# Optimization experiments

Hardware: AMD Instinct MI355X
Metric: run time of the kernel (lower is better)

The kernel has to match this reference:

```python
import jax, jax.numpy as jnp
import numpy as np

NUM_CLASSES = 80
IMG = 640
STRIDES = (8, 16, 32)
CENTER_RADIUS = 2.5
TOPK = 10  # n_candidate_k; dynamic_ks = clamp(int(sum top-10 IoU), 1) <= 10


def _make_grids():
    gs, ss = [], []
    for s in STRIDES:
        n = IMG // s
        gy, gx = np.meshgrid(np.arange(n), np.arange(n), indexing="ij")
        gs.append(np.stack([gx.ravel(), gy.ravel()], 1).astype(np.float32))
        ss.append(np.full(n * n, s, np.float32))
    return np.concatenate(gs, 0), np.concatenate(ss, 0)


def setup_inputs() -> dict:
    key = jax.random.key(0)
    B, T, C = 16, 128, NUM_CLASSES
    grid_np, stride_np = _make_grids()
    A = grid_np.shape[0]  # 8400
    k1, k2, k3, k4, k5, k6 = jax.random.split(key, 6)
    # pred boxes: plausible abs xyxy around anchor centers
    ctr = jnp.asarray((grid_np + 0.5) * stride_np[:, None])[None]
    ctr = ctr + 4.0 * jax.random.normal(k1, (B, A, 2))
    wh = jnp.asarray(stride_np)[None, :, None] * jax.random.uniform(k2, (B, A, 2), minval=1.0, maxval=4.0)
    box = jnp.concatenate([ctr - wh / 2, ctr + wh / 2], -1)
    logits = 2.0 * jax.random.normal(k3, (B, A, 1 + C))
    pred = jnp.concatenate([box, logits], -1)  # [B, A, 5+C]
    # targets: [B, T, 6] = (batch_id, cid, x1, y1, x2, y2)
    tc = jax.random.uniform(k4, (B, T, 2), minval=60.0, maxval=580.0)
    twh = jax.random.uniform(k5, (B, T, 2), minval=30.0, maxval=200.0)
    tbox = jnp.concatenate([tc - twh / 2, tc + twh / 2], -1)
    cid = jax.random.randint(k6, (B, T, 1), 0, C).astype(jnp.float32)
    bid = jnp.broadcast_to(jnp.arange(B, dtype=jnp.float32)[:, None, None], (B, T, 1))
    target = jnp.concatenate([bid, cid, tbox], -1)
    return {"pred": pred, "target": target,
            "grid_mask": jnp.asarray(grid_np), "stride_mask": jnp.asarray(stride_np)}


def _pairwise_iou(a, b):
    # a [T,4], b [A,4], xyxy -> [T,A]
    lt = jnp.maximum(a[:, None, :2], b[None, :, :2])
    rb = jnp.minimum(a[:, None, 2:], b[None, :, 2:])
    wh = jnp.clip(rb - lt, 0.0, None)
    inter = wh[..., 0] * wh[..., 1]
    area_a = jnp.clip(a[:, 2] - a[:, 0], 0.0, None) * jnp.clip(a[:, 3] - a[:, 1], 0.0, None)
    area_b = jnp.clip(b[:, 2] - b[:, 0], 0.0, None) * jnp.clip(b[:, 3] - b[:, 1], 0.0, None)
    return inter / (area_a[:, None] + area_b[None, :] - inter + 1e-8)


def _ciou(p, t):
    # complete IoU, elementwise over leading dims, xyxy
    lt = jnp.maximum(p[..., :2], t[..., :2])
    rb = jnp.minimum(p[..., 2:], t[..., 2:])
    wh = jnp.clip(rb - lt, 0.0, None)
    inter = wh[..., 0] * wh[..., 1]
    wp, hp = p[..., 2] - p[..., 0], p[..., 3] - p[..., 1]
    wt, ht = t[..., 2] - t[..., 0], t[..., 3] - t[..., 1]
    iou = inter / (wp * hp + wt * ht - inter + 1e-8)
    cwh = jnp.maximum(p[..., 2:], t[..., 2:]) - jnp.minimum(p[..., :2], t[..., :2])
    c2 = cwh[..., 0] ** 2 + cwh[..., 1] ** 2 + 1e-8
    rho2 = (((p[..., 0] + p[..., 2]) - (t[..., 0] + t[..., 2])) ** 2
            + ((p[..., 1] + p[..., 3]) - (t[..., 1] + t[..., 3])) ** 2) / 4.0
    v = (4.0 / jnp.pi ** 2) * (jnp.arctan(wt / (ht + 1e-8)) - jnp.arctan(wp / (hp + 1e-8))) ** 2
    alpha = v / (1.0 - iou + v + 1e-8)
    return iou - rho2 / c2 - alpha * v


def _bce_logits(x, t):
    return jnp.maximum(x, 0.0) - x * t + jnp.log1p(jnp.exp(-jnp.abs(x)))


def _assign_image(pred_i, tgt_i, grid, stride):
    # pred_i [A,5+C], tgt_i [T,6]
    A, T, C = pred_i.shape[0], tgt_i.shape[0], NUM_CLASSES
    tbox = tgt_i[:, 2:6]
    cid = tgt_i[:, 1].astype(jnp.int32)
    xc = (grid[:, 0] + 0.5) * stride  # [A]
    yc = (grid[:, 1] + 0.5) * stride
    d = jnp.stack([xc[None] - tbox[:, 0:1], yc[None] - tbox[:, 1:2],
                   tbox[:, 2:3] - xc[None], tbox[:, 3:4] - yc[None]], -1)  # [T,A,4]
    in_boxes = d.min(-1) > 0.0  # [T,A]
    txc = (tbox[:, 0] + tbox[:, 2]) / 2
    tyc = (tbox[:, 1] + tbox[:, 3]) / 2
    in_centers = jnp.maximum(jnp.abs(xc[None] - txc[:, None]),
                             jnp.abs(yc[None] - tyc[:, None])) < CENTER_RADIUS * stride[None]
    in_box = in_boxes.any(0) | in_centers.any(0)  # [A], candidate anchors
    in_box_center = in_boxes & in_centers  # [T,A]
    iou = jnp.where(in_box[None], _pairwise_iou(tbox, pred_i[:, :4]), 0.0)  # [T,A]
    iou_cost = -jnp.log(iou + 1e-8)
    prob = jnp.sqrt(jax.nn.sigmoid(pred_i[:, 4:5]) * jax.nn.sigmoid(pred_i[:, 5:]))  # [A,C]
    logp = jnp.maximum(jnp.log(prob), -100.0)      # torch BCE clamps log at -100
    log1mp = jnp.maximum(jnp.log1p(-prob), -100.0)
    # sum_c BCE(prob, onehot(cid)) computed analytically (avoids [T,A,C]):
    cls_cost = -(log1mp.sum(-1)[None, :] + (logp - log1mp)[:, cid].T)  # [T,A]
    # 1e9 keeps anchors outside in_box out of the candidate pool (original slices them away)
    cost = cls_cost + 3.0 * iou_cost + 1e5 * (~in_box_center) + 1e9 * (~in_box)[None, :]
    topk_ious, _ = jax.lax.top_k(iou, TOPK)  # [T,10]
    dyn_k = jnp.maximum(topk_ious.sum(1).astype(jnp.int32), 1)  # [T]
    _, idx = jax.lax.top_k(-cost, TOPK)  # 10 lowest-cost anchors per target
    sel = jnp.arange(TOPK)[None, :] < dyn_k[:, None]  # keep first dyn_k of them
    matching = jnp.zeros((T, A), bool).at[jnp.arange(T)[:, None], idx].set(sel)
    matching = matching & in_box[None, :]
    conflict = matching.sum(0) > 1  # anchors claimed by >1 targets
    keep = jnp.arange(T)[:, None] == jnp.argmin(cost, 0)[None, :]  # [T,A]
    matching = jnp.where(conflict[None, :], keep, matching)
    mp = matching.any(0)  # [A]
    tp = jnp.argmax(matching, 0)  # [A] target index per anchor
    p_iou = jnp.clip((iou / (iou.max(1, keepdims=True) + 1e-8)).max(0), 0.0, 1.0)  # [A]
    obj_t = jnp.where(in_box, p_iou, 0.0)
    box_t = tbox[tp]  # [A,4]
    cls_t = jax.nn.one_hot(cid[tp], C, dtype=jnp.float32)  # [A,C]
    return mp, box_t, obj_t, cls_t


def reference(pred, target, grid_mask, stride_mask):
    B, A = pred.shape[:2]
    C = NUM_CLASSES
    mp, box_t, obj_t, cls_t = jax.lax.stop_gradient(
        jax.vmap(_assign_image, in_axes=(0, 0, None, None))(pred, target, grid_mask, stride_mask))
    m = mp.reshape(-1).astype(pred.dtype)  # matched-anchor mask over B*A
    n = jnp.maximum(m.sum(), 1.0)
    p = pred.reshape(B * A, -1)
    lbox = 0.05 * jnp.sum((1.0 - _ciou(p[:, :4], box_t.reshape(-1, 4))) * m) / n
    lobj = _bce_logits(p[:, 4], obj_t.reshape(-1)).mean()
    lcls = 0.5 * jnp.sum(_bce_logits(p[:, 5:], cls_t.reshape(-1, C)).mean(-1) * m) / n
    loss = lbox + lobj + lcls
    return loss, jnp.stack([lbox, lobj, lcls])
```

## Files before the change

### kernel.cpp

```cpp
#include <hip/hip_runtime.h>
#include <cfloat>

#pragma clang fp contract(off)

#define NCLS 80
#define PDIM 85
#define NA   8400
#define NAP  8448
#define NB   16
#define NT   128
#define NTOP 10
#define APB  64
#define BPI  132
#define BPI2 33
#define LN2  0.6931471805599453f
#define CAPW 768

#define BAPC ((size_t)NB*NAP)

#define KSENT 0xFFFFFFFF7FFFFFFFull

__device__ __forceinline__ float sigm_fast(float x){
  float e = __expf(-x);
  return __builtin_amdgcn_rcpf(1.0f + e);
}

__device__ __forceinline__ float bce_fast(float x, float t){
  float ax = fabsf(x);
  float e  = __expf(-ax);
  return fmaxf(x,0.0f) - x*t + LN2*__builtin_amdgcn_logf(1.0f + e);
}

__device__ __forceinline__ float pair_iou(float tx1,float ty1,float tx2,float ty2,
                                          float px1,float py1,float px2,float py2){
  float w = fminf(tx2,px2) - fmaxf(tx1,px1);
  float h = fminf(ty2,py2) - fmaxf(ty1,py1);
  w = fmaxf(w,0.0f); h = fmaxf(h,0.0f);
  float inter = w*h;
  float at = fmaxf(tx2-tx1,0.0f)*fmaxf(ty2-ty1,0.0f);
  float ap = fmaxf(px2-px1,0.0f)*fmaxf(py2-py1,0.0f);
  float den = at+ap-inter+1e-8f;
  return inter * __builtin_amdgcn_rcpf(den);
}

__device__ __forceinline__ float dval_fn(float sobj, float lg){
  float ln_sobj = LN2*__builtin_amdgcn_logf(sobj);
  float e = __expf(-fabsf(lg));
  float L = LN2*__builtin_amdgcn_logf(1.0f + e);
  float ln_sc = -(fmaxf(-lg,0.0f) + L);
  float lph = 0.5f*(ln_sobj + ln_sc);
  float p = __expf(lph);
  float lp = fmaxf(lph, -100.0f);
  float l1 = fmaxf(LN2*__builtin_amdgcn_logf(fmaxf(1.0f - p, 0.0f)), -100.0f);
  return lp - l1;
}

__device__ __forceinline__ float cost_from(float S, float dval, float iou, bool ibc, bool ib){
  float iouc = -LN2 * __builtin_amdgcn_logf(iou + 1e-8f);
  float clsc = -(S + dval);
  float c = clsc + 3.0f*iouc;
  c = c + (ibc ? 0.0f : 100000.0f);
  c = c + (ib  ? 0.0f : 1000000000.0f);
  return c;
}

__device__ __forceinline__ unsigned long long key_of(float c, int idx){
  unsigned int u = __float_as_uint(c);
  u ^= (u & 0x80000000u) ? 0xFFFFFFFFu : 0x80000000u;
  return ((unsigned long long)u << 32) | (unsigned int)idx;
}

__device__ __forceinline__ void ins_iou(float* riou, float iou){
  if (iou > riou[NTOP-1]){
    #pragma unroll
    for (int j = NTOP-1; j >= 1; --j){
      bool gj  = iou > riou[j];
      bool gj1 = iou > riou[j-1];
      riou[j] = gj ? (gj1 ? riou[j-1] : iou) : riou[j];
    }
    riou[0] = (iou > riou[0]) ? iou : riou[0];
  }
}
__device__ __forceinline__ void ins_key(unsigned long long* rk, unsigned long long key){
  if (key < rk[NTOP-1]){
    #pragma unroll
    for (int j = NTOP-1; j >= 1; --j){
      bool bj  = key < rk[j];
      bool bj1 = key < rk[j-1];
      rk[j] = bj ? (bj1 ? rk[j-1] : key) : rk[j];
    }
    rk[0] = (key < rk[0]) ? key : rk[0];
  }
}

__global__ __launch_bounds__(256) void k0_precompute(
    const float* __restrict__ pred, const float* __restrict__ target,
    const float* __restrict__ grid, const float* __restrict__ stridev,
    float4* __restrict__ pbox4, float4* __restrict__ meta4,
    float* __restrict__ obja, float* __restrict__ sobja,
    float* __restrict__ S0a, float* __restrict__ D, int use_d,
    unsigned long long* __restrict__ mask, unsigned int* __restrict__ obju,
    float4* __restrict__ gaabb, unsigned long long* __restrict__ actm,
    float* __restrict__ acc)
{
  __shared__ __align__(16) float tile[APB*PDIM];
  __shared__ float4 tb4s[NT];
  __shared__ float  ps_s[4][APB];
  __shared__ float  ps0_s[4][APB];
  __shared__ int    ib_s[4][APB];

  int i  = blockIdx.x / BPI;
  int b  = blockIdx.x % BPI;
  int c0 = b*APB;
  int n  = NA - c0; if (n > APB) n = APB;
  int tid = threadIdx.x;

  if (blockIdx.x == 0) acc[tid] = 0.0f;

  const float4* src4 = (const float4*)(pred + ((size_t)i*NA + c0)*PDIM);
  int tot4 = (n*PDIM) >> 2;
  for (int idx = tid; idx < tot4; idx += 256) ((float4*)tile)[idx] = src4[idx];
  for (int idx = tid; idx < NT; idx += 256){
    const float* tg = target + (i*NT + idx)*6;
    tb4s[idx] = make_float4(tg[2],tg[3],tg[4],tg[5]);
  }
  __syncthreads();

  int al = tid & 63, cg = tid >> 6;
  if (al < n){
    int gid = i*NAP + c0 + al;
    float x4 = tile[al*PDIM+4];
    float e4 = __expf(-fabsf(x4));
    float L4 = LN2*__builtin_amdgcn_logf(1.0f + e4);
    float ln_sobj = -(fmaxf(-x4,0.0f) + L4);
    float ps = 0.0f, ps0 = 0.0f;
    #pragma unroll 4
    for (int k = 0; k < 20; ++k){
      int c = cg*20 + k;
      float x  = tile[al*PDIM+5+c];
      float e  = __expf(-fabsf(x));
      float L  = LN2*__builtin_amdgcn_logf(1.0f + e);
      float ln_sc = -(fmaxf(-x,0.0f) + L);
      float lph = 0.5f*(ln_sobj + ln_sc);
      float p   = __expf(lph);
      float lp  = fmaxf(lph, -100.0f);
      float l1  = fmaxf(LN2*__builtin_amdgcn_logf(fmaxf(1.0f - p, 0.0f)), -100.0f);
      ps  += l1;
      if (use_d) D[(size_t)c*BAPC + gid] = lp - l1;
      ps0 += fmaxf(x,0.0f) + L;
    }
    ps_s[cg][al] = ps; ps0_s[cg][al] = ps0;

    int ga = c0 + al;
    float xg = grid[2*ga], yg = grid[2*ga+1], sv = stridev[ga];
    float xc = (xg + 0.5f)*sv, yc = (yg + 0.5f)*sv;
    float rc = 2.5f*sv;
    bool ibp = false;
    #pragma unroll 4
    for (int t = cg*32; t < cg*32+32; ++t){
      float4 T = tb4s[t];
      bool inb = (xc-T.x>0.0f)&&(yc-T.y>0.0f)&&(T.z-xc>0.0f)&&(T.w-yc>0.0f);
      float txc=(T.x+T.z)*0.5f, tyc=(T.y+T.w)*0.5f;
      bool inc = fmaxf(fabsf(xc-txc),fabsf(yc-tyc)) < rc;
      ibp = ibp || inb || inc;
    }
    ib_s[cg][al] = ibp ? 1 : 0;
  }
  __syncthreads();

  if (tid < APB){
    int a = tid;
    bool real = (a < n);
    int gid = i*NAP + c0 + a;
    float x1=0,y1=0,x2=0,y2=0,xc=0,yc=0,rc=0;
    bool ib = false;

    if (real){
      float s  = ps_s[0][a]  + ps_s[1][a]  + ps_s[2][a]  + ps_s[3][a];
      float s0 = ps0_s[0][a] + ps0_s[1][a] + ps0_s[2][a] + ps0_s[3][a];
      ib  = (ib_s[0][a] | ib_s[1][a] | ib_s[2][a] | ib_s[3][a]) != 0;

      x1 = tile[a*PDIM+0]; y1 = tile[a*PDIM+1];
      x2 = tile[a*PDIM+2]; y2 = tile[a*PDIM+3];
      float ol = tile[a*PDIM+4];
      pbox4[gid] = make_float4(x1,y1,x2,y2);
      obja[gid]  = ol;
      sobja[gid] = sigm_fast(ol);
      S0a[gid]   = s0;
      mask[(size_t)gid*2]   = 0ull;
      mask[(size_t)gid*2+1] = 0ull;
      obju[gid] = 0u;

      int ga = c0 + a;
      float xg = grid[2*ga], yg = grid[2*ga+1], sv = stridev[ga];
      xc = (xg + 0.5f)*sv; yc = (yg + 0.5f)*sv;
      rc = 2.5f*sv;
      meta4[gid] = make_float4(xc, yc, ib ? rc : -rc, s);
    } else {
      meta4[gid] = make_float4(0.0f, 0.0f, -1.0f, 0.0f);
      pbox4[gid] = make_float4(0.0f, 0.0f, 0.0f, 0.0f);
      obju[gid]  = 0u;
    }

    bool iv = real && ib;
    unsigned long long am = __ballot(iv);
    float bx1 = iv ? x1 : FLT_MAX,  by1 = iv ? y1 : FLT_MAX;
    float bx2 = iv ? x2 : -FLT_MAX, by2 = iv ? y2 : -FLT_MAX;
    float cx1 = iv ? xc : FLT_MAX,  cy1 = iv ? yc : FLT_MAX;
    float cx2 = iv ? xc : -FLT_MAX, cy2 = iv ? yc : -FLT_MAX;
    float rx1 = iv ? xc-rc : FLT_MAX,  ry1 = iv ? yc-rc : FLT_MAX;
    float rx2 = iv ? xc+rc : -FLT_MAX, ry2 = iv ? yc+rc : -FLT_MAX;
    #pragma unroll
    for (int off = 32; off > 0; off >>= 1){
      bx1 = fminf(bx1, __shfl_xor(bx1, off));
      by1 = fminf(by1, __shfl_xor(by1, off));
      bx2 = fmaxf(bx2, __shfl_xor(bx2, off));
      by2 = fmaxf(by2, __shfl_xor(by2, off));
      cx1 = fminf(cx1, __shfl_xor(cx1, off));
      cy1 = fminf(cy1, __shfl_xor(cy1, off));
      cx2 = fmaxf(cx2, __shfl_xor(cx2, off));
      cy2 = fmaxf(cy2, __shfl_xor(cy2, off));
      rx1 = fminf(rx1, __shfl_xor(rx1, off));
      ry1 = fminf(ry1, __shfl_xor(ry1, off));
      rx2 = fmaxf(rx2, __shfl_xor(rx2, off));
      ry2 = fmaxf(ry2, __shfl_xor(ry2, off));
    }
    if (tid == 0){
      size_t gb = (size_t)(i*BPI + b)*3;
      gaabb[gb+0] = make_float4(bx1,by1,bx2,by2);
      gaabb[gb+1] = make_float4(cx1,cy1,cx2,cy2);
      gaabb[gb+2] = make_float4(rx1,ry1,rx2,ry2);
      actm[i*BPI + b] = am;
    }
  }
}

__global__ __launch_bounds__(256) void k1_pertarget(
    const float4* __restrict__ pbox4, const float4* __restrict__ meta4,
    const float* __restrict__ D, int use_d,
    const float* __restrict__ sobja, const float* __restrict__ pred,
    const float* __restrict__ target, const float4* __restrict__ gaabb,
    const unsigned long long* __restrict__ actm,
    unsigned int* __restrict__ obju, unsigned long long* __restrict__ mask)
{
  __shared__ int   seg[4*CAPW];
  __shared__ int   cnts_s[4], cibc_s[4];
  __shared__ float wiou[4][NTOP];
  __shared__ unsigned long long wkey[4][NTOP];
  __shared__ float rmax_s;

  int tid = threadIdx.x, lane = tid & 63, w = tid >> 6;
  int g = blockIdx.x;
  int i = g / NT, t = g - i*NT;
  int iNAP = i*NAP;
  int iNA  = i*NA;
  const float* m4f = (const float*)meta4;

  const float* tg = target + (size_t)g*6;
  int   cid = (int)tg[1];
  float tx1 = tg[2], ty1 = tg[3], tx2 = tg[4], ty2 = tg[5];
  float txc = (tx1+tx2)*0.5f, tyc = (ty1+ty2)*0.5f;
  const float* Dc = use_d ? (D + (size_t)cid*BAPC) : nullptr;

  bool sv = false, svi = false;
  if (lane < 33){
    size_t gb = (size_t)(i*BPI + (w + 4*lane))*3;
    float4 gbb = gaabb[gb+0];
    float4 gcc = gaabb[gb+1];
    float4 grr = gaabb[gb+2];
    bool ovg  = (fminf(tx2,gbb.z) > fmaxf(tx1,gbb.x)) &&
                (fminf(ty2,gbb.w) > fmaxf(ty1,gbb.y));
    bool inbg = (gcc.z > tx1) && (gcc.x < tx2) && (gcc.w > ty1) && (gcc.y < ty2);
    bool incg = (txc > grr.x) && (txc < grr.z) && (tyc > grr.y) && (tyc < grr.w);
    svi = inbg && incg;
    sv = ovg || svi;
  }
  unsigned long long gmsk  = __ballot(sv);
  unsigned long long gmski = __ballot(svi);

  int cnt = 0, ci = 0;
  while (gmsk){
    int k = __ffsll(gmsk) - 1;
    unsigned long long kb = 1ull << k;
    gmsk &= gmsk - 1;
    int a = w*64 + k*256 + lane;
    float4 pb = pbox4[iNAP+a];

    bool ov  = (fminf(tx2,pb.z) > fmaxf(tx1,pb.x)) &&
               (fminf(ty2,pb.w) > fmaxf(ty1,pb.y));

    if (gmski & kb){
      float4 mt = meta4[iNAP+a];
      bool act = (mt.z > 0.0f);
      bool inb = (mt.x-tx1>0.0f)&&(mt.y-ty1>0.0f)&&(tx2-mt.x>0.0f)&&(ty2-mt.y>0.0f);
      bool inc = fmaxf(fabsf(mt.x-txc),fabsf(mt.y-tyc)) < mt.z;
      bool ibc = inb && inc;
      bool cand = act && (ov || ibc);
      unsigned long long bb  = __ballot(cand);
      unsigned long long bb2 = __ballot(ibc);
      if (cand){
        int pos = cnt + __popcll(bb & ((1ull << lane) - 1ull));
        if (pos < CAPW) seg[w*CAPW + pos] = a | (ibc ? (1<<15) : 0);
      }
      cnt += __popcll(bb);
      ci  += __popcll(bb2);
    } else {
      unsigned long long am = actm[i*BPI + (w + 4*k)];
      bool act = (am >> lane) & 1ull;
      bool cand = act && ov;
      unsigned long long bb = __ballot(cand);
      if (cand){
        int pos = cnt + __popcll(bb & ((1ull << lane) - 1ull));
        if (pos < CAPW) seg[w*CAPW + pos] = a;
      }
      cnt += __popcll(bb);
    }
  }
  if (lane == 0){ cnts_s[w] = cnt; cibc_s[w] = ci; }
  __syncthreads();

  int tibc = cibc_s[0]+cibc_s[1]+cibc_s[2]+cibc_s[3];
  bool ovf = (cnts_s[0]>CAPW)||(cnts_s[1]>CAPW)||(cnts_s[2]>CAPW)||(cnts_s[3]>CAPW);
  bool fastp = !ovf && (tibc >= 16);

  float riou[NTOP]; unsigned long long rk[NTOP];
  #pragma unroll
  for (int j=0;j<NTOP;++j){ riou[j]=0.0f; rk[j]=KSENT; }

  int cw = cnts_s[w];
  if (fastp){
    for (int j = lane; j < cw; j += 64){
      int e  = seg[w*CAPW + j];
      int a1 = e & 0x3fff;
      bool ibc = (e & (1<<15)) != 0;
      int gid = iNAP + a1;
      float4 pb2 = pbox4[gid];
      float iou = pair_iou(tx1,ty1,tx2,ty2, pb2.x,pb2.y,pb2.z,pb2.w);
      ins_iou(riou, iou);
      float S  = m4f[(size_t)gid*4 + 3];
      float dv = use_d ? Dc[gid] : dval_fn(sobja[gid], pred[(size_t)(iNA+a1)*PDIM + 5 + cid]);
      float c  = cost_from(S, dv, iou, ibc, true);
      ins_key(rk, key_of(c, a1));
    }
  } else {
    for (int a1 = tid; a1 < NA; a1 += 256){
      float4 mt2 = meta4[iNAP+a1];
      if (mt2.z > 0.0f){
        float4 pb2 = pbox4[iNAP+a1];
        float iou = pair_iou(tx1,ty1,tx2,ty2, pb2.x,pb2.y,pb2.z,pb2.w);
        ins_iou(riou, iou);
        bool inb = (mt2.x-tx1>0.0f)&&(mt2.y-ty1>0.0f)&&(tx2-mt2.x>0.0f)&&(ty2-mt2.y>0.0f);
        bool inc = fmaxf(fabsf(mt2.x-txc),fabsf(mt2.y-tyc)) < mt2.z;
        float dv = use_d ? Dc[iNAP+a1] : dval_fn(sobja[iNAP+a1], pred[(size_t)(iNA+a1)*PDIM + 5 + cid]);
        float c = cost_from(mt2.w, dv, iou, inb&&inc, true);
        ins_key(rk, key_of(c, a1));
      }
    }
  }

  #pragma unroll
  for (int r = 0; r < NTOP; ++r){
    float gm = riou[0];
    #pragma unroll
    for (int m = 1; m < 64; m <<= 1) gm = fmaxf(gm, __shfl_xor(gm, m));
    unsigned long long bb = __ballot(riou[0] == gm);
    int win = __ffsll(bb) - 1;
    if (lane == win){
      #pragma unroll
      for (int j=0;j<NTOP-1;++j) riou[j] = riou[j+1];
      riou[NTOP-1] = 0.0f;
    }
    if (lane == 0) wiou[w][r] = gm;
  }
  #pragma unroll
  for (int r = 0; r < NTOP; ++r){
    unsigned long long gk = rk[0];
    #pragma unroll
    for (int m = 1; m < 64; m <<= 1){
      unsigned long long o = __shfl_xor(gk, m);
      gk = (o < gk) ? o : gk;
    }
    if (rk[0] == gk){
      #pragma unroll
      for (int j=0;j<NTOP-1;++j) rk[j] = rk[j+1];
      rk[NTOP-1] = KSENT;
    }
    if (lane == 0) wkey[w][r] = gk;
  }
  __syncthreads();

  int dk = 1;
  if (w == 0){
    int p0=0,p1=0,p2=0,p3=0;
    float ssum = 0.0f, rmax = 0.0f;
    #pragma unroll
    for (int r = 0; r < NTOP; ++r){
      float v0=wiou[0][p0], v1=wiou[1][p1], v2=wiou[2][p2], v3=wiou[3][p3];
      float mx = fmaxf(fmaxf(v0,v1), fmaxf(v2,v3));
      if (r == 0) rmax = mx;
      ssum += mx;
      if      (mx == v0) ++p0;
      else if (mx == v1) ++p1;
      else if (mx == v2) ++p2;
      else               ++p3;
    }
    dk = (int)ssum;
    if (dk < 1) dk = 1;
    if (lane == 0) rmax_s = rmax;
  }
  __syncthreads();

  float invm = 1.0f / (rmax_s + 1e-8f);
  if (fastp){
    for (int j = lane; j < cw; j += 64){
      int a1 = seg[w*CAPW + j] & 0x3fff;
      int gid = iNAP + a1;
      float4 pb2 = pbox4[gid];
      float iou = pair_iou(tx1,ty1,tx2,ty2, pb2.x,pb2.y,pb2.z,pb2.w);
      float v = iou * invm;
      if (v > 0.0f) atomicMax(&obju[gid], __float_as_uint(v));
    }
  } else {
    for (int a1 = tid; a1 < NA; a1 += 256){
      float4 mt2 = meta4[iNAP+a1];
      if (mt2.z > 0.0f){
        float4 pb2 = pbox4[iNAP+a1];
        float iou = pair_iou(tx1,ty1,tx2,ty2, pb2.x,pb2.y,pb2.z,pb2.w);
        float v = iou * invm;
        if (v > 0.0f) atomicMax(&obju[iNAP+a1], __float_as_uint(v));
      }
    }
  }

  if (w == 0){
    int q0=0,q1=0,q2=0,q3=0;
    int myidx = 0x7fffffff;
    #pragma unroll
    for (int r = 0; r < NTOP; ++r){
      unsigned long long k0=wkey[0][q0], k1=wkey[1][q1], k2=wkey[2][q2], k3=wkey[3][q3];
      unsigned long long mn = k0;
      mn = (k1 < mn) ? k1 : mn;
      mn = (k2 < mn) ? k2 : mn;
      mn = (k3 < mn) ? k3 : mn;
      if (lane == r) myidx = (int)(mn & 0xFFFFFFFFull);
      if      (mn == k0) ++q0;
      else if (mn == k1) ++q1;
      else if (mn == k2) ++q2;
      else               ++q3;
    }

    if (lane < NTOP && lane < dk){
      int a1 = myidx;
      if (a1 >= 0 && a1 < NA){
        atomicOr(&mask[(size_t)(iNAP + a1)*2 + (t>>6)], 1ull << (t & 63));
      }
    }
  }
}

__global__ __launch_bounds__(256) void k2_peranchor(
    const float* __restrict__ pred,
    const float4* __restrict__ pbox4, const float4* __restrict__ meta4,
    const float* __restrict__ obja, const float* __restrict__ sobja,
    const float* __restrict__ S0a,
    const float* __restrict__ D, int use_d,
    const float* __restrict__ target,
    const unsigned int* __restrict__ obju, const unsigned long long* __restrict__ mask,
    float* __restrict__ acc)
{
  __shared__ float4 tb4[NT];
  __shared__ int    tcid[NT];
  __shared__ int    cl[256];
  __shared__ int    bt_s[256];
  __shared__ int    ncl;
  __shared__ float4 part[4];

  int i  = blockIdx.x / BPI2;
  int b  = blockIdx.x - i*BPI2;
  int tid = threadIdx.x, lane = tid & 63, w = tid >> 6;
  int a  = b*256 + tid;
  int gid = i*NAP + a;

  if (tid < NT){
    const float* tg = target + (i*NT + tid)*6;
    tcid[tid] = (int)tg[1];
    tb4[tid]  = make_float4(tg[2],tg[3],tg[4],tg[5]);
  }
  if (tid == 0) ncl = 0;

  bool valid = (a < NA);
  float4 pb = pbox4[gid];
  float4 mt = meta4[gid];
  unsigned long long m0=0, m1=0;
  if (valid){ m0 = mask[(size_t)gid*2]; m1 = mask[(size_t)gid*2+1]; }
  float bestv = __uint_as_float(obju[gid]);
  float olv   = obja[gid];
  float S0v   = S0a[gid];

  bool ib = valid && (mt.z > 0.0f);
  float px1=pb.x, py1=pb.y, px2=pb.z, py2=pb.w;
  int cnt = __popcll(m0) + __popcll(m1);

  __syncthreads();

  bool myc = (cnt > 1);
  unsigned long long cb = __ballot(myc);
  int nb = __popcll(cb);
  int base = 0;
  if (lane == 0 && nb) base = atomicAdd(&ncl, nb);
  base = __shfl(base, 0);
  if (myc) cl[base + __popcll(cb & ((1ull << lane) - 1ull))] = tid;
  __syncthreads();

  int tot = ncl;
  for (int ci = w; ci < tot; ci += 4){
    int aidx = cl[ci];
    int a2g  = b*256 + aidx;
    int gid2 = i*NAP + a2g;
    float4 pb2 = pbox4[gid2];
    float4 mt2 = meta4[gid2];
    bool ib2 = (mt2.z > 0.0f);
    float rc2 = fabsf(mt2.z);
    float Sg  = mt2.w;
    float sobj = use_d ? 0.0f : sobja[gid2];
    size_t pbase = (size_t)(i*NA + a2g)*PDIM;

    int ta = lane, tb = lane + 64;
    float dva = use_d ? D[(size_t)tcid[ta]*BAPC + gid2]
                      : dval_fn(sobj, pred[pbase + 5 + tcid[ta]]);
    float dvb = use_d ? D[(size_t)tcid[tb]*BAPC + gid2]
                      : dval_fn(sobj, pred[pbase + 5 + tcid[tb]]);

    float4 Ta = tb4[ta];
    float ioua = ib2 ? pair_iou(Ta.x,Ta.y,Ta.z,Ta.w,pb2.x,pb2.y,pb2.z,pb2.w) : 0.0f;
    bool inba = (mt2.x-Ta.x>0.0f)&&(mt2.y-Ta.y>0.0f)&&(Ta.z-mt2.x>0.0f)&&(Ta.w-mt2.y>0.0f);
    float txa=(Ta.x+Ta.z)*0.5f, tya=(Ta.y+Ta.w)*0.5f;
    bool inca = fmaxf(fabsf(mt2.x-txa),fabsf(mt2.y-tya)) < rc2;
    unsigned long long ka = key_of(cost_from(Sg, dva, ioua, inba&&inca, ib2), ta);

    float4 Tb = tb4[tb];
    float ioub = ib2 ? pair_iou(Tb.x,Tb.y,Tb.z,Tb.w,pb2.x,pb2.y,pb2.z,pb2.w) : 0.0f;
    bool inbb = (mt2.x-Tb.x>0.0f)&&(mt2.y-Tb.y>0.0f)&&(Tb.z-mt2.x>0.0f)&&(Tb.w-mt2.y>0.0f);
    float txb=(Tb.x+Tb.z)*0.5f, tyb=(Tb.y+Tb.w)*0.5f;
    bool incb = fmaxf(fabsf(mt2.x-txb),fabsf(mt2.y-tyb)) < rc2;
    unsigned long long kb = key_of(cost_from(Sg, dvb, ioub, inbb&&incb, ib2), tb);

    unsigned long long mn = (kb < ka) ? kb : ka;
    #pragma unroll
    for (int m = 1; m < 64; m <<= 1){
      unsigned long long o = __shfl_xor(mn, m);
      mn = (o < mn) ? o : mn;
    }
    if (lane == 0) bt_s[aidx] = (int)(mn & 0xFFFFFFFFull);
  }
  __syncthreads();

  float m=0.0f, vbox=0.0f, vobj=0.0f, vcls=0.0f;
  if (valid){
    float obj_t = ib ? fminf(fmaxf(bestv,0.0f),1.0f) : 0.0f;
    vobj = bce_fast(olv, obj_t);

    int tp = 0; bool mpv = false;
    if (cnt > 1){ tp = bt_s[tid]; mpv = true; }
    else if (cnt == 1){
      tp = m0 ? (__ffsll(m0)-1) : (64 + __ffsll(m1)-1);
      mpv = true;
    }

    if (mpv){
      m = 1.0f;
      float4 T = tb4[tp];
      float x1=T.x, y1=T.y, x2=T.z, y2=T.w;
      float w2 = fmaxf(fminf(px2,x2)-fmaxf(px1,x1),0.0f);
      float h2 = fmaxf(fminf(py2,y2)-fmaxf(py1,y1),0.0f);
      float inter = w2*h2;
      float wp=px2-px1, hp=py2-py1, wt=x2-x1, ht=y2-y1;
      float iou = inter/(wp*hp + wt*ht - inter + 1e-8f);
      float cw = fmaxf(px2,x2)-fminf(px1,x1);
      float ch = fmaxf(py2,y2)-fminf(py1,y1);
      float c2 = cw*cw + ch*ch + 1e-8f;
      float dx = (px1+px2)-(x1+x2), dy = (py1+py2)-(y1+y2);
      float rho2 = (dx*dx + dy*dy)/4.0f;
      float da = atanf(wt/(ht+1e-8f)) - atanf(wp/(hp+1e-8f));
      float v  = 0.4052847345693511f * da * da;
      float alpha = v/(1.0f - iou + v + 1e-8f);
      vbox = 1.0f - (iou - rho2/c2 - alpha*v);

      int cc = tcid[tp];
      float xcc = pred[(size_t)(i*NA + a)*PDIM + 5 + cc];
      vcls = (S0v - xcc) * (1.0f/80.0f);
    }
  }

  #pragma unroll
  for (int off=32; off>0; off>>=1){
    m    += __shfl_down(m, off);
    vbox += __shfl_down(vbox, off);
    vobj += __shfl_down(vobj, off);
    vcls += __shfl_down(vcls, off);
  }
  if (lane == 0) part[w] = make_float4(m, vbox, vobj, vcls);
  __syncthreads();
  if (tid == 0){
    float4 s0 = part[0], s1 = part[1], s2 = part[2], s3 = part[3];
    float4 s = make_float4(s0.x+s1.x+s2.x+s3.x, s0.y+s1.y+s2.y+s3.y,
                           s0.z+s1.z+s2.z+s3.z, s0.w+s1.w+s2.w+s3.w);
    int slot = (blockIdx.x & 63)*4;
    atomicAdd(&acc[slot+0], s.x);
    atomicAdd(&acc[slot+1], s.y);
    atomicAdd(&acc[slot+2], s.z);
    atomicAdd(&acc[slot+3], s.w);
  }
}

__global__ void k3_final(const float* __restrict__ acc, float* __restrict__ out){
  int l = threadIdx.x;
  float4 v = ((const float4*)acc)[l];
  #pragma unroll
  for (int off=32; off>0; off>>=1){
    v.x += __shfl_down(v.x, off);
    v.y += __shfl_down(v.y, off);
    v.z += __shfl_down(v.z, off);
    v.w += __shfl_down(v.w, off);
  }
  if (l == 0){
    float n    = fmaxf(v.x, 1.0f);
    float lbox = 0.05f * v.y / n;
    float lobj = v.z / (float)(NB*NA);
    float lcls = 0.5f  * v.w / n;
    out[0] = lbox + lobj + lcls;
    out[1] = lbox; out[2] = lobj; out[3] = lcls;
  }
}

extern "C" void kernel_launch(void* const* d_in, const int* in_sizes, int n_in,
                              void* d_out, int out_size, void* d_ws, size_t ws_size,
                              hipStream_t stream) {
  const float* pred    = (const float*)d_in[0];
  const float* target  = (const float*)d_in[1];
  const float* grid    = (const float*)d_in[2];
  const float* stridev = (const float*)d_in[3];
  float* out = (float*)d_out;

  char* ws = (char*)d_ws;

  size_t off = 0;
  unsigned long long* mask = (unsigned long long*)(ws + off); off += BAPC*16;
  float* acc    = (float*)(ws + off); off += 64*4*4;
  float4* pbox4 = (float4*)(ws + off); off += BAPC*16;
  float4* meta4 = (float4*)(ws + off); off += BAPC*16;
  float* obja   = (float*)(ws + off); off += BAPC*4;
  float* sobja  = (float*)(ws + off); off += BAPC*4;
  float* S0a    = (float*)(ws + off); off += BAPC*4;
  unsigned int* obju = (unsigned int*)(ws + off); off += BAPC*4;
  float4* gaabb = (float4*)(ws + off); off += (size_t)NB*BPI*3*16;
  unsigned long long* actm = (unsigned long long*)(ws + off); off += (size_t)NB*BPI*8;
  float* D      = (float*)(ws + off);
  const size_t need_d = off + (size_t)NCLS*BAPC*4;
  int use_d = (ws_size >= need_d) ? 1 : 0;

  k0_precompute<<<NB*BPI, 256, 0, stream>>>(pred, target, grid, stridev,
                                            pbox4, meta4, obja, sobja, S0a, D, use_d,
                                            mask, obju, gaabb, actm, acc);
  k1_pertarget <<<NB*NT,  256, 0, stream>>>(pbox4, meta4, D, use_d,
                                            sobja, pred, target, gaabb, actm,
                                            obju, mask);
  k2_peranchor <<<NB*BPI2, 256, 0, stream>>>(pred, pbox4, meta4, obja, sobja, S0a,
                                             D, use_d, target, obju, mask, acc);
  k3_final     <<<1, 64, 0, stream>>>(acc, out);
}
```

Baseline: 152.6 us.

## Drop precomputed per-class D table and recompute cost terms on demand

Removes the large per-class D array that k0 wrote for every anchor and class (80×B×A floats) and the sigmoid-objectness buffer. k1 and k2 now recompute the class cost term from the raw objectness and class logit via a log-sigmoid formulation. k1 also caches the candidate IoU in shared memory (int2 segment) so the second pass skips reloading boxes and recomputing IoU, with the per-warp capacity reduced from 768 to 512 to keep shared memory in check. This trades large global writes for extra transcendental math, and the smaller capacity may push more targets onto the slow path.

```diff
diff --git a/kernel.cpp b/kernel.cpp
--- a/kernel.cpp
+++ b/kernel.cpp
@@ -14,16 +14,11 @@
 #define BPI  132
 #define BPI2 33
 #define LN2  0.6931471805599453f
-#define CAPW 768
+#define CAPW 512
 
 #define BAPC ((size_t)NB*NAP)
 
 #define KSENT 0xFFFFFFFF7FFFFFFFull
-
-__device__ __forceinline__ float sigm_fast(float x){
-  float e = __expf(-x);
-  return __builtin_amdgcn_rcpf(1.0f + e);
-}
 
 __device__ __forceinline__ float bce_fast(float x, float t){
   float ax = fabsf(x);
@@ -43,15 +38,17 @@
   return inter * __builtin_amdgcn_rcpf(den);
 }
 
-__device__ __forceinline__ float dval_fn(float sobj, float lg){
-  float ln_sobj = LN2*__builtin_amdgcn_logf(sobj);
-  float e = __expf(-fabsf(lg));
-  float L = LN2*__builtin_amdgcn_logf(1.0f + e);
+__device__ __forceinline__ float dval_exact(float ol, float lg){
+  float e4 = __expf(-fabsf(ol));
+  float L4 = LN2*__builtin_amdgcn_logf(1.0f + e4);
+  float ln_sobj = -(fmaxf(-ol,0.0f) + L4);
+  float e  = __expf(-fabsf(lg));
+  float L  = LN2*__builtin_amdgcn_logf(1.0f + e);
   float ln_sc = -(fmaxf(-lg,0.0f) + L);
   float lph = 0.5f*(ln_sobj + ln_sc);
-  float p = __expf(lph);
-  float lp = fmaxf(lph, -100.0f);
-  float l1 = fmaxf(LN2*__builtin_amdgcn_logf(fmaxf(1.0f - p, 0.0f)), -100.0f);
+  float p   = __expf(lph);
+  float lp  = fmaxf(lph, -100.0f);
+  float l1  = fmaxf(LN2*__builtin_amdgcn_logf(fmaxf(1.0f - p, 0.0f)), -100.0f);
   return lp - l1;
 }
 
@@ -97,8 +94,7 @@
     const float* __restrict__ pred, const float* __restrict__ target,
     const float* __restrict__ grid, const float* __restrict__ stridev,
     float4* __restrict__ pbox4, float4* __restrict__ meta4,
-    float* __restrict__ obja, float* __restrict__ sobja,
-    float* __restrict__ S0a, float* __restrict__ D, int use_d,
+    float* __restrict__ obja, float* __restrict__ S0a,
     unsigned long long* __restrict__ mask, unsigned int* __restrict__ obju,
     float4* __restrict__ gaabb, unsigned long long* __restrict__ actm,
     float* __restrict__ acc)
@@ -128,7 +124,6 @@
 
   int al = tid & 63, cg = tid >> 6;
   if (al < n){
-    int gid = i*NAP + c0 + al;
     float x4 = tile[al*PDIM+4];
     float e4 = __expf(-fabsf(x4));
     float L4 = LN2*__builtin_amdgcn_logf(1.0f + e4);
@@ -143,10 +138,8 @@
       float ln_sc = -(fmaxf(-x,0.0f) + L);
       float lph = 0.5f*(ln_sobj + ln_sc);
       float p   = __expf(lph);
-      float lp  = fmaxf(lph, -100.0f);
       float l1  = fmaxf(LN2*__builtin_amdgcn_logf(fmaxf(1.0f - p, 0.0f)), -100.0f);
       ps  += l1;
-      if (use_d) D[(size_t)c*BAPC + gid] = lp - l1;
       ps0 += fmaxf(x,0.0f) + L;
     }
     ps_s[cg][al] = ps; ps0_s[cg][al] = ps0;
@@ -185,7 +178,6 @@
       float ol = tile[a*PDIM+4];
       pbox4[gid] = make_float4(x1,y1,x2,y2);
       obja[gid]  = ol;
-      sobja[gid] = sigm_fast(ol);
       S0a[gid]   = s0;
       mask[(size_t)gid*2]   = 0ull;
       mask[(size_t)gid*2+1] = 0ull;
@@ -237,13 +229,12 @@
 
 __global__ __launch_bounds__(256) void k1_pertarget(
     const float4* __restrict__ pbox4, const float4* __restrict__ meta4,
-    const float* __restrict__ D, int use_d,
-    const float* __restrict__ sobja, const float* __restrict__ pred,
+    const float* __restrict__ obja, const float* __restrict__ pred,
     const float* __restrict__ target, const float4* __restrict__ gaabb,
     const unsigned long long* __restrict__ actm,
     unsigned int* __restrict__ obju, unsigned long long* __restrict__ mask)
 {
-  __shared__ int   seg[4*CAPW];
+  __shared__ int2  seg2[4*CAPW];
   __shared__ int   cnts_s[4], cibc_s[4];
   __shared__ float wiou[4][NTOP];
   __shared__ unsigned long long wkey[4][NTOP];
@@ -260,7 +251,6 @@
   int   cid = (int)tg[1];
   float tx1 = tg[2], ty1 = tg[3], tx2 = tg[4], ty2 = tg[5];
   float txc = (tx1+tx2)*0.5f, tyc = (ty1+ty2)*0.5f;
-  const float* Dc = use_d ? (D + (size_t)cid*BAPC) : nullptr;
 
   bool sv = false, svi = false;
   if (lane < 33){
@@ -300,7 +290,7 @@
       unsigned long long bb2 = __ballot(ibc);
       if (cand){
         int pos = cnt + __popcll(bb & ((1ull << lane) - 1ull));
-        if (pos < CAPW) seg[w*CAPW + pos] = a | (ibc ? (1<<15) : 0);
+        if (pos < CAPW) seg2[w*CAPW + pos].x = a | (ibc ? (1<<15) : 0);
       }
       cnt += __popcll(bb);
       ci  += __popcll(bb2);
@@ -311,7 +301,7 @@
       unsigned long long bb = __ballot(cand);
       if (cand){
         int pos = cnt + __popcll(bb & ((1ull << lane) - 1ull));
-        if (pos < CAPW) seg[w*CAPW + pos] = a;
+        if (pos < CAPW) seg2[w*CAPW + pos].x = a;
       }
       cnt += __popcll(bb);
     }
@@ -330,15 +320,16 @@
   int cw = cnts_s[w];
   if (fastp){
     for (int j = lane; j < cw; j += 64){
-      int e  = seg[w*CAPW + j];
+      int e  = seg2[w*CAPW + j].x;
       int a1 = e & 0x3fff;
       bool ibc = (e & (1<<15)) != 0;
       int gid = iNAP + a1;
       float4 pb2 = pbox4[gid];
       float iou = pair_iou(tx1,ty1,tx2,ty2, pb2.x,pb2.y,pb2.z,pb2.w);
+      seg2[w*CAPW + j].y = __float_as_int(iou);
       ins_iou(riou, iou);
       float S  = m4f[(size_t)gid*4 + 3];
-      float dv = use_d ? Dc[gid] : dval_fn(sobja[gid], pred[(size_t)(iNA+a1)*PDIM + 5 + cid]);
+      float dv = dval_exact(obja[gid], pred[(size_t)(iNA+a1)*PDIM + 5 + cid]);
       float c  = cost_from(S, dv, iou, ibc, true);
       ins_key(rk, key_of(c, a1));
     }
@@ -351,7 +342,7 @@
         ins_iou(riou, iou);
         bool inb = (mt2.x-tx1>0.0f)&&(mt2.y-ty1>0.0f)&&(tx2-mt2.x>0.0f)&&(ty2-mt2.y>0.0f);
         bool inc = fmaxf(fabsf(mt2.x-txc),fabsf(mt2.y-tyc)) < mt2.z;
-        float dv = use_d ? Dc[iNAP+a1] : dval_fn(sobja[iNAP+a1], pred[(size_t)(iNA+a1)*PDIM + 5 + cid]);
+        float dv = dval_exact(obja[iNAP+a1], pred[(size_t)(iNA+a1)*PDIM + 5 + cid]);
         float c = cost_from(mt2.w, dv, iou, inb&&inc, true);
         ins_key(rk, key_of(c, a1));
       }
@@ -413,12 +404,11 @@
   float invm = 1.0f / (rmax_s + 1e-8f);
   if (fastp){
     for (int j = lane; j < cw; j += 64){
-      int a1 = seg[w*CAPW + j] & 0x3fff;
-      int gid = iNAP + a1;
-      float4 pb2 = pbox4[gid];
-      float iou = pair_iou(tx1,ty1,tx2,ty2, pb2.x,pb2.y,pb2.z,pb2.w);
+      int2 e = seg2[w*CAPW + j];
+      int a1 = e.x & 0x3fff;
+      float iou = __int_as_float(e.y);
       float v = iou * invm;
-      if (v > 0.0f) atomicMax(&obju[gid], __float_as_uint(v));
+      if (v > 0.0f) atomicMax(&obju[iNAP + a1], __float_as_uint(v));
     }
   } else {
     for (int a1 = tid; a1 < NA; a1 += 256){
@@ -461,9 +451,7 @@
 __global__ __launch_bounds__(256) void k2_peranchor(
     const float* __restrict__ pred,
     const float4* __restrict__ pbox4, const float4* __restrict__ meta4,
-    const float* __restrict__ obja, const float* __restrict__ sobja,
-    const float* __restrict__ S0a,
-    const float* __restrict__ D, int use_d,
+    const float* __restrict__ obja, const float* __restrict__ S0a,
     const float* __restrict__ target,
     const unsigned int* __restrict__ obju, const unsigned long long* __restrict__ mask,
     float* __restrict__ acc)
@@ -522,14 +510,12 @@
     bool ib2 = (mt2.z > 0.0f);
     float rc2 = fabsf(mt2.z);
     float Sg  = mt2.w;
-    float sobj = use_d ? 0.0f : sobja[gid2];
+    float ol2 = obja[gid2];
     size_t pbase = (size_t)(i*NA + a2g)*PDIM;
 
     int ta = lane, tb = lane + 64;
-    float dva = use_d ? D[(size_t)tcid[ta]*BAPC + gid2]
-                      : dval_fn(sobj, pred[pbase + 5 + tcid[ta]]);
-    float dvb = use_d ? D[(size_t)tcid[tb]*BAPC + gid2]
-                      : dval_fn(sobj, pred[pbase + 5 + tcid[tb]]);
+    float dva = dval_exact(ol2, pred[pbase + 5 + tcid[ta]]);
+    float dvb = dval_exact(ol2, pred[pbase + 5 + tcid[tb]]);
 
     float4 Ta = tb4[ta];
     float ioua = ib2 ? pair_iou(Ta.x,Ta.y,Ta.z,Ta.w,pb2.x,pb2.y,pb2.z,pb2.w) : 0.0f;
@@ -650,22 +636,17 @@
   float4* pbox4 = (float4*)(ws + off); off += BAPC*16;
   float4* meta4 = (float4*)(ws + off); off += BAPC*16;
   float* obja   = (float*)(ws + off); off += BAPC*4;
-  float* sobja  = (float*)(ws + off); off += BAPC*4;
   float* S0a    = (float*)(ws + off); off += BAPC*4;
   unsigned int* obju = (unsigned int*)(ws + off); off += BAPC*4;
   float4* gaabb = (float4*)(ws + off); off += (size_t)NB*BPI*3*16;
   unsigned long long* actm = (unsigned long long*)(ws + off); off += (size_t)NB*BPI*8;
-  float* D      = (float*)(ws + off);
-  const size_t need_d = off + (size_t)NCLS*BAPC*4;
-  int use_d = (ws_size >= need_d) ? 1 : 0;
 
   k0_precompute<<<NB*BPI, 256, 0, stream>>>(pred, target, grid, stridev,
-                                            pbox4, meta4, obja, sobja, S0a, D, use_d,
+                                            pbox4, meta4, obja, S0a,
                                             mask, obju, gaabb, actm, acc);
-  k1_pertarget <<<NB*NT,  256, 0, stream>>>(pbox4, meta4, D, use_d,
-                                            sobja, pred, target, gaabb, actm,
-                                            obju, mask);
-  k2_peranchor <<<NB*BPI2, 256, 0, stream>>>(pred, pbox4, meta4, obja, sobja, S0a,
-                                             D, use_d, target, obju, mask, acc);
+  k1_pertarget <<<NB*NT,  256, 0, stream>>>(pbox4, meta4, obja, pred, target,
+                                            gaabb, actm, obju, mask);
+  k2_peranchor <<<NB*BPI2, 256, 0, stream>>>(pred, pbox4, meta4, obja, S0a,
+                                             target, obju, mask, acc);
   k3_final     <<<1, 64, 0, stream>>>(acc, out);
 }
```

New measurement: 155.0 us. About the same (+1.6%).
